# Performance work log

Measured on AMD Instinct MI355X. Metric: run time of the kernel, lower is better.

## Reference

```python
import jax, jax.numpy as jnp
import numpy as np

TOTAL = 16777216  # total nodes across all graphs
N = 65536         # number of graphs (len(v_count))
K = 16            # k_pool


def setup_inputs() -> dict:
    key = jax.random.key(0)
    k1, k2 = jax.random.split(key)
    Y = jax.random.normal(k1, (TOTAL, 1), dtype=jnp.float32)
    W = jnp.ones((K,), dtype=jnp.float32)  # initializer Ones, as in build()
    e_map = jnp.sort(jax.random.randint(k2, (TOTAL,), 0, N, dtype=jnp.int32))
    v_count = jnp.ones((N,), dtype=jnp.int32)  # only its length is used
    return {"Y": Y, "W": W, "e_map": e_map, "v_count": v_count}


def reference(Y, W, e_map, v_count):
    # Faithful SortPooling forward. Instead of materializing the padded
    # [N, max_seg_len] -inf tensor, we do k_pool fused segment-max passes:
    # each pass extracts the current per-segment max and masks out exactly
    # one occurrence (the first, by index) -- identical to tf.math.top_k on
    # the -inf-padded ragged-to-dense tensor (ties yield duplicate values,
    # matching top_k semantics).
    n = v_count.shape[0]
    k = W.shape[0]  # static k_pool; segments here are much larger than k
    y = jnp.squeeze(Y, axis=-1)  # [TOTAL]
    total = y.shape[0]
    idxs = jnp.arange(total, dtype=jnp.int32)
    neg_inf = jnp.float32(-jnp.inf)

    y_work = y
    tops = []
    for _ in range(k):
        m = jax.ops.segment_max(y_work, e_map, num_segments=n)  # [N]
        tops.append(m)
        is_max = y_work == m[e_map]
        # first index attaining the max in each segment (total == sentinel)
        first = jax.ops.segment_min(jnp.where(is_max, idxs, total),
                                    e_map, num_segments=n)  # [N]
        # OOB indices (exhausted/empty segments) are dropped by scatter
        y_work = y_work.at[first].set(neg_inf)

    Y_top = jnp.stack(tops, axis=-1)        # [N, k] sorted descending
    Wn = jax.nn.softmax(W)                  # [k]
    Y_w = jnp.where(jnp.isinf(Y_top), jnp.float32(0.0), Y_top) * Wn
    return jnp.sum(Y_w, axis=-1)            # [N]
```

## Files before the change

### kernel.cpp

```cpp
#include <hip/hip_runtime.h>
#include <math.h>

#define KPOOL 16
#define SPLIT 8

__device__ __forceinline__ void ce(float& x, float& y) {
  float hi = fmaxf(x, y), lo = fminf(x, y);
  x = hi;
  y = lo;
}

__device__ __forceinline__ void sort8(float (&v)[8]) {
  ce(v[0], v[1]); ce(v[2], v[3]); ce(v[4], v[5]); ce(v[6], v[7]);
  ce(v[0], v[2]); ce(v[1], v[3]); ce(v[4], v[6]); ce(v[5], v[7]);
  ce(v[1], v[2]); ce(v[5], v[6]);
  ce(v[0], v[4]); ce(v[1], v[5]); ce(v[2], v[6]); ce(v[3], v[7]);
  ce(v[2], v[4]); ce(v[3], v[5]);
  ce(v[1], v[2]); ce(v[3], v[4]); ce(v[5], v[6]);
}

__device__ __forceinline__ void merge8into16(float (&t)[KPOOL], const float (&b)[8]) {
#pragma unroll
  for (int i = 8; i < 16; ++i) t[i] = fmaxf(t[i], b[15 - i]);
#pragma unroll
  for (int s = 8; s >= 1; s >>= 1) {
#pragma unroll
    for (int i = 0; i < 16; ++i)
      if ((i & s) == 0) ce(t[i], t[i + s]);
  }
}

__device__ __forceinline__ void merge_partner(float (&t)[KPOOL], int dist) {
  float c[KPOOL];
#pragma unroll
  for (int i = 0; i < KPOOL; ++i) {
    float o = __shfl_xor(t[KPOOL - 1 - i], dist);
    c[i] = fmaxf(t[i], o);
  }
#pragma unroll
  for (int s = 8; s >= 1; s >>= 1) {
#pragma unroll
    for (int i = 0; i < KPOOL; ++i)
      if ((i & s) == 0) ce(c[i], c[i + s]);
  }
#pragma unroll
  for (int i = 0; i < KPOOL; ++i) t[i] = c[i];
}

__device__ __forceinline__ int lower_bound_range(const int* __restrict__ a,
                                                 int lo, int hi, int key) {
  while (lo < hi) {
    int mid = (lo + hi) >> 1;
    if (a[mid] < key) lo = mid + 1;
    else hi = mid;
  }
  return lo;
}

__global__ __launch_bounds__(256)
void boundary_kernel(const int* __restrict__ emap, int total, int n,
                     int* __restrict__ starts, float* __restrict__ wn_out,
                     const float* __restrict__ W) {
  int g = blockIdx.x * 256 + threadIdx.x;
  if (g == 0) {
    float w[KPOOL], m = -INFINITY, s = 0.0f;
#pragma unroll
    for (int k = 0; k < KPOOL; ++k) { w[k] = W[k]; m = fmaxf(m, w[k]); }
#pragma unroll
    for (int k = 0; k < KPOOL; ++k) { w[k] = expf(w[k] - m); s += w[k]; }
#pragma unroll
    for (int k = 0; k < KPOOL; ++k) wn_out[k] = w[k] / s;
  }
  if (g > n) return;
  long long E = (long long)g * total / n;
  int wlo = (int)(E - 8192 > 0 ? E - 8192 : 0);
  int whi = (int)(E + 8192 < total ? E + 8192 : total);
  bool ok = ((wlo == 0) || (emap[wlo - 1] < g)) &&
            ((whi == total) || (emap[whi] >= g));
  if (!ok) { wlo = 0; whi = total; }
  starts[g] = lower_bound_range(emap, wlo, whi, g);
}

__global__ __launch_bounds__(256, 4)
void sortpool_main(const float* __restrict__ Y, const float* __restrict__ W,
                   const int* __restrict__ starts, const float* __restrict__ Wn,
                   const int* __restrict__ emap,
                   float* __restrict__ out, int total, int n) {
  const int tid = blockIdx.x * 256 + threadIdx.x;
  const int g = tid >> 3;
  const int q = tid & 7;
  if (g >= n) return;

  int s0, s1;
  if (starts) {
    s0 = starts[g];
    s1 = starts[g + 1];
  } else {
    s0 = lower_bound_range(emap, 0, total, g);
    s1 = lower_bound_range(emap, 0, total, g + 1);
  }
  const unsigned len = (unsigned)(s1 - s0);

  const int B0 = s0 >> 3;
  const int B1 = (s1 + 7) >> 3;

  float t[KPOOL];
#pragma unroll
  for (int i = 0; i < KPOOL; ++i) t[i] = -INFINITY;

  int b = B0 + q;
  float4 n0, n1;
  if (b < B1) {
    const float4* p = reinterpret_cast<const float4*>(Y + (b << 3));
    n0 = p[0];
    n1 = p[1];
  }
#pragma unroll 1
  while (b < B1) {
    const float4 c0 = n0, c1 = n1;
    const int base = b << 3;
    const int bn = b + SPLIT;
    if (bn < B1) {
      const float4* p = reinterpret_cast<const float4*>(Y + (bn << 3));
      n0 = p[0];
      n1 = p[1];
    }
    float v[8] = {c0.x, c0.y, c0.z, c0.w, c1.x, c1.y, c1.z, c1.w};
#pragma unroll
    for (int j = 0; j < 8; ++j) {
      if ((unsigned)(base + j - s0) >= len) v[j] = -INFINITY;
    }
    sort8(v);
    merge8into16(t, v);
    b = bn;
  }

  merge_partner(t, 1);
  merge_partner(t, 2);
  merge_partner(t, 4);

  float res = 0.0f;
  if (Wn) {
#pragma unroll
    for (int k = 0; k < KPOOL; ++k) {
      float tv = t[k];
      res += (tv > -INFINITY) ? tv * Wn[k] : 0.0f;
    }
  } else {
    float wv[KPOOL], m = -INFINITY, s = 0.0f;
#pragma unroll
    for (int k = 0; k < KPOOL; ++k) { wv[k] = W[k]; m = fmaxf(m, wv[k]); }
#pragma unroll
    for (int k = 0; k < KPOOL; ++k) { wv[k] = expf(wv[k] - m); s += wv[k]; }
    const float inv = 1.0f / s;
#pragma unroll
    for (int k = 0; k < KPOOL; ++k) {
      float tv = t[k];
      res += (tv > -INFINITY) ? tv * (wv[k] * inv) : 0.0f;
    }
  }

  if (q == 0) out[g] = res;
}

extern "C" void kernel_launch(void* const* d_in, const int* in_sizes, int n_in,
                              void* d_out, int out_size, void* d_ws, size_t ws_size,
                              hipStream_t stream) {
  const float* Y = (const float*)d_in[0];
  const float* W = (const float*)d_in[1];
  const int* emap = (const int*)d_in[2];
  const int total = in_sizes[0];
  const int n = in_sizes[3];
  float* out = (float*)d_out;

  int* starts = (int*)d_ws;
  float* wn_buf = (float*)((char*)d_ws + (size_t)(n + 1) * sizeof(int));
  const bool use_ws =
      (ws_size >= (size_t)(n + 1) * sizeof(int) + KPOOL * sizeof(float));

  if (use_ws) {
    int nb = (n + 1 + 255) / 256;
    boundary_kernel<<<nb, 256, 0, stream>>>(emap, total, n, starts, wn_buf, W);
  }

  long long threads = (long long)n * SPLIT;
  int blocks = (int)((threads + 255) / 256);
  sortpool_main<<<blocks, 256, 0, stream>>>(Y, W, use_ws ? starts : nullptr,
                                            use_ws ? wn_buf : nullptr,
                                            emap, out, total, n);
}
```

Before: 36.26 us.

## Halve threads per segment, deepen prefetch to two blocks, use nontemporal loads

Each graph segment is now handled by 4 threads instead of 8, which drops one cross-lane merge stage. The load pipeline now keeps two 8-float blocks in flight instead of one, and Y is read with nontemporal loads to avoid polluting the cache. The intent is to cut merge overhead and hide memory latency better. In exchange each thread walks a longer serial loop, there are fewer threads overall, and register pressure goes up.

After: 40.92 us. +12.9%, slower.

```diff
diff --git a/kernel.cpp b/kernel.cpp
--- a/kernel.cpp
+++ b/kernel.cpp
@@ -2,7 +2,9 @@
 #include <math.h>
 
 #define KPOOL 16
-#define SPLIT 8
+#define SPLIT 4
+
+typedef float f32x4 __attribute__((ext_vector_type(4)));
 
 __device__ __forceinline__ void ce(float& x, float& y) {
   float hi = fmaxf(x, y), lo = fminf(x, y);
@@ -87,8 +89,8 @@
                    const int* __restrict__ emap,
                    float* __restrict__ out, int total, int n) {
   const int tid = blockIdx.x * 256 + threadIdx.x;
-  const int g = tid >> 3;
-  const int q = tid & 7;
+  const int g = tid >> 2;
+  const int q = tid & 3;
   if (g >= n) return;
 
   int s0, s1;
@@ -109,35 +111,41 @@
   for (int i = 0; i < KPOOL; ++i) t[i] = -INFINITY;
 
   int b = B0 + q;
-  float4 n0, n1;
+  int bn = b + SPLIT;
+  f32x4 c0 = 0, c1 = 0, n0 = 0, n1 = 0;
   if (b < B1) {
-    const float4* p = reinterpret_cast<const float4*>(Y + (b << 3));
-    n0 = p[0];
-    n1 = p[1];
+    const f32x4* p = reinterpret_cast<const f32x4*>(Y + (b << 3));
+    c0 = __builtin_nontemporal_load(p);
+    c1 = __builtin_nontemporal_load(p + 1);
   }
-#pragma unroll 1
+  if (bn < B1) {
+    const f32x4* p = reinterpret_cast<const f32x4*>(Y + (bn << 3));
+    n0 = __builtin_nontemporal_load(p);
+    n1 = __builtin_nontemporal_load(p + 1);
+  }
+#pragma unroll 2
   while (b < B1) {
-    const float4 c0 = n0, c1 = n1;
+    const int b2 = bn + SPLIT;
+    f32x4 p0 = 0, p1 = 0;
+    if (b2 < B1) {
+      const f32x4* p = reinterpret_cast<const f32x4*>(Y + (b2 << 3));
+      p0 = __builtin_nontemporal_load(p);
+      p1 = __builtin_nontemporal_load(p + 1);
+    }
     const int base = b << 3;
-    const int bn = b + SPLIT;
-    if (bn < B1) {
-      const float4* p = reinterpret_cast<const float4*>(Y + (bn << 3));
-      n0 = p[0];
-      n1 = p[1];
-    }
-    float v[8] = {c0.x, c0.y, c0.z, c0.w, c1.x, c1.y, c1.z, c1.w};
+    float v[8] = {c0[0], c0[1], c0[2], c0[3], c1[0], c1[1], c1[2], c1[3]};
 #pragma unroll
     for (int j = 0; j < 8; ++j) {
       if ((unsigned)(base + j - s0) >= len) v[j] = -INFINITY;
     }
     sort8(v);
     merge8into16(t, v);
-    b = bn;
+    c0 = n0; c1 = n1; n0 = p0; n1 = p1;
+    b = bn; bn = b2;
   }
 
   merge_partner(t, 1);
   merge_partner(t, 2);
-  merge_partner(t, 4);
 
   float res = 0.0f;
   if (Wn) {
```
